# Kernel tuning notes

Hardware: AMD Instinct MI355X
Metric: run time of the kernel (lower is better)

## Reference

```python
import jax, jax.numpy as jnp
import numpy as np

H, DK = 16, 64
D = H * DK  # d_model = 1024
B, S = 2, 2048


def setup_inputs() -> dict:
    key = jax.random.key(0)
    ks = jax.random.split(key, 11)
    std = 1.0 / np.sqrt(D)
    inp = {
        "query": jax.random.normal(ks[0], (B, S, D), dtype=jnp.float32),
        "key": jax.random.normal(ks[1], (B, S, D), dtype=jnp.float32),
        "value": jax.random.normal(ks[2], (B, S, D), dtype=jnp.float32),
        "Wq": jax.random.normal(ks[3], (D, D), dtype=jnp.float32) * std,
        "bq": jnp.zeros((D,), dtype=jnp.float32),
        "Wk": jax.random.normal(ks[4], (D, D), dtype=jnp.float32) * std,
        "bk": jnp.zeros((D,), dtype=jnp.float32),
        "Wv": jax.random.normal(ks[5], (D, D), dtype=jnp.float32) * std,
        "bv": jnp.zeros((D,), dtype=jnp.float32),
        "Wo": jax.random.normal(ks[6], (D, D), dtype=jnp.float32) * std,
        "bo": jnp.zeros((D,), dtype=jnp.float32),
    }
    return inp


def reference(query, key, value, Wq, bq, Wk, bk, Wv, bv, Wo, bo):
    # torch.nn.Linear convention: y = x @ W.T + b
    def split_heads(x):
        b, s, _ = x.shape
        return x.reshape(b, s, H, DK).transpose(0, 2, 1, 3)  # [B,H,S,DK]

    q = split_heads(query @ Wq.T + bq)
    k = split_heads(key @ Wk.T + bk)
    v = split_heads(value @ Wv.T + bv)

    scale = 1.0 / jnp.sqrt(jnp.asarray(DK, dtype=q.dtype))
    scores = jnp.einsum("bhqd,bhkd->bhqk", q, k) * scale  # [B,H,S,S]
    p_attn = jax.nn.softmax(scores, axis=-1)
    ctx = jnp.einsum("bhqk,bhkd->bhqd", p_attn, v)  # [B,H,S,DK]

    ctx = ctx.transpose(0, 2, 1, 3).reshape(query.shape[0], -1, H * DK)
    return ctx @ Wo.T + bo
```

## Files before the change

### kernel.cpp

```cpp
#include <hip/hip_runtime.h>
#include <stdint.h>

#define BATCH 2
#define SEQ   2048
#define NHEAD 16
#define DK    64
#define DMODEL 1024
#define MROWS (BATCH*SEQ)

typedef __attribute__((ext_vector_type(8))) __bf16 bf16x8;
typedef __attribute__((ext_vector_type(4))) float f32x4;
typedef __attribute__((ext_vector_type(8))) unsigned short u16x8;
typedef __attribute__((ext_vector_type(4))) unsigned short u16x4;

#define QSCALE 0.18033688f

__device__ __forceinline__ unsigned short f2bf(float f) {
  union { float f; uint32_t u; } c; c.f = f;
  uint32_t u = c.u;
  return (unsigned short)((u + 0x7fffu + ((u >> 16) & 1u)) >> 16);
}

__device__ __forceinline__ void gld16(const void* g, void* lds) {
  __builtin_amdgcn_global_load_lds(
      (const __attribute__((address_space(1))) void*)g,
      (__attribute__((address_space(3))) void*)lds,
      16, 0, 0);
}

__global__ __launch_bounds__(256)
void cvt_all(const float* __restrict__ q, const float* __restrict__ k, const float* __restrict__ v,
             const float* __restrict__ Wq, const float* __restrict__ Wk,
             const float* __restrict__ Wv, const float* __restrict__ Wo,
             unsigned short* __restrict__ Xq, unsigned short* __restrict__ Xk,
             unsigned short* __restrict__ Xv,
             unsigned short* __restrict__ Wqb, unsigned short* __restrict__ Wkb,
             unsigned short* __restrict__ Wvb, unsigned short* __restrict__ Wob) {
  int blk = blockIdx.x;
  const float* in; unsigned short* out; int base;
  if (blk < 6144) {
    int ti = blk >> 11;
    in  = (ti == 0) ? q  : (ti == 1) ? k  : v;
    out = (ti == 0) ? Xq : (ti == 1) ? Xk : Xv;
    base = (blk & 2047) * 2048;
  } else {
    int ti = (blk - 6144) >> 9;
    in  = (ti == 0) ? Wq  : (ti == 1) ? Wk  : (ti == 2) ? Wv  : Wo;
    out = (ti == 0) ? Wqb : (ti == 1) ? Wkb : (ti == 2) ? Wvb : Wob;
    base = ((blk - 6144) & 511) * 2048;
  }
  int i = base + threadIdx.x * 8;
  float4 a = *(const float4*)(in + i);
  float4 b = *(const float4*)(in + i + 4);
  u16x8 o;
  o[0]=f2bf(a.x); o[1]=f2bf(a.y); o[2]=f2bf(a.z); o[3]=f2bf(a.w);
  o[4]=f2bf(b.x); o[5]=f2bf(b.y); o[6]=f2bf(b.z); o[7]=f2bf(b.w);
  *(u16x8*)(out + i) = o;
}

template <int MODE, int MT>
__device__ __forceinline__ void gemm_body(unsigned short* __restrict__ lA,
                                          unsigned short* __restrict__ lB,
                                          const unsigned short* __restrict__ X,
                                          const unsigned short* __restrict__ W,
                                          const float* __restrict__ bias,
                                          unsigned short* __restrict__ Yb,
                                          float* __restrict__ Yf,
                                          int rowBase, int colBase) {
  const int t = threadIdx.x;
  const int lane = t & 63, wave = t >> 6;
  const int cl = lane & 15, qd = lane >> 4;
  const int wm = wave >> 1, wn = wave & 1;
  const int srow = t >> 3, sslot = t & 7;

  int aoff[2][MT], boff[2][4];
  #pragma unroll
  for (int ks = 0; ks < 2; ks++) {
    #pragma unroll
    for (int i = 0; i < MT; i++) {
      int ra = wm * (MT * 16) + i * 16 + cl;
      aoff[ks][i] = ra * 64 + ((ks * 4 + qd) ^ (ra & 7)) * 8;
    }
    #pragma unroll
    for (int i = 0; i < 4; i++) {
      int rb = wn * 64 + i * 16 + cl;
      boff[ks][i] = rb * 64 + ((ks * 4 + qd) ^ (rb & 7)) * 8;
    }
  }
  const unsigned short* xp[MT];
  const unsigned short* wp[4];
  #pragma unroll
  for (int i = 0; i < MT; i++) {
    int r = i * 32 + srow;
    int chunk = sslot ^ (r & 7);
    xp[i] = X + (size_t)(rowBase + r) * DMODEL + chunk * 8;
  }
  #pragma unroll
  for (int i = 0; i < 4; i++) {
    int r = i * 32 + srow;
    int chunk = sslot ^ (r & 7);
    wp[i] = W + (size_t)(colBase + r) * DMODEL + chunk * 8;
  }

  f32x4 zero = {0.f, 0.f, 0.f, 0.f};
  f32x4 acc[MT][4];
  for (int mt = 0; mt < MT; mt++) for (int nt = 0; nt < 4; nt++) acc[mt][nt] = zero;

  for (int k0 = 0; k0 < DMODEL; k0 += 64) {
    __syncthreads();
    #pragma unroll
    for (int i = 0; i < MT; i++) {
      gld16(xp[i], (char*)lA + i * 4096 + wave * 1024);
      xp[i] += 64;
    }
    #pragma unroll
    for (int i = 0; i < 4; i++) {
      gld16(wp[i], (char*)lB + i * 4096 + wave * 1024);
      wp[i] += 64;
    }
    __syncthreads();
    #pragma unroll
    for (int ks = 0; ks < 2; ks++) {
      bf16x8 af[MT], bfr[4];
      #pragma unroll
      for (int mt = 0; mt < MT; mt++) af[mt] = *(const bf16x8*)&lA[aoff[ks][mt]];
      #pragma unroll
      for (int nt = 0; nt < 4; nt++) bfr[nt] = *(const bf16x8*)&lB[boff[ks][nt]];
      #pragma unroll
      for (int mt = 0; mt < MT; mt++)
        #pragma unroll
        for (int nt = 0; nt < 4; nt++) {
          if (MODE == 2)
            acc[mt][nt] = __builtin_amdgcn_mfma_f32_16x16x32_bf16(af[mt], bfr[nt], acc[mt][nt], 0, 0, 0);
          else
            acc[mt][nt] = __builtin_amdgcn_mfma_f32_16x16x32_bf16(bfr[nt], af[mt], acc[mt][nt], 0, 0, 0);
        }
    }
  }

  if (MODE == 2) {
    #pragma unroll
    for (int mt = 0; mt < MT; mt++) {
      int row0 = rowBase + wm * (MT * 16) + mt * 16 + qd * 4;
      int bb = row0 >> 11;
      int s_in = row0 & 2047;
      int blk = s_in & ~63;
      int n4 = (s_in & 63) >> 2;
      int l4 = n4 & 7;
      int pos = 8 * (n4 >> 3) + ((l4 < 4) ? 2 * l4 : 2 * (l4 - 4) + 1);
      #pragma unroll
      for (int nt = 0; nt < 4; nt++) {
        int c = colBase + wn * 64 + nt * 16 + cl;
        float bv = bias[c];
        int hh = c >> 6, d = c & 63;
        u16x4 v;
        #pragma unroll
        for (int r = 0; r < 4; r++) v[r] = f2bf(acc[mt][nt][r] + bv);
        *(u16x4*)&Yb[(size_t)((bb * NHEAD + hh) * 64 + d) * SEQ + blk + pos * 4] = v;
      }
    }
  } else {
    #pragma unroll
    for (int nt = 0; nt < 4; nt++) {
      int col = colBase + wn * 64 + nt * 16 + qd * 4;
      f32x4 bv4 = *(const f32x4*)&bias[col];
      #pragma unroll
      for (int mt = 0; mt < MT; mt++) {
        int row = rowBase + wm * (MT * 16) + mt * 16 + cl;
        if (MODE == 3) {
          f32x4 v;
          #pragma unroll
          for (int r = 0; r < 4; r++) v[r] = acc[mt][nt][r] + bv4[r];
          *(f32x4*)&Yf[(size_t)row * DMODEL + col] = v;
        } else {
          u16x4 v;
          #pragma unroll
          for (int r = 0; r < 4; r++) {
            float x = acc[mt][nt][r] + bv4[r];
            v[r] = f2bf(MODE == 1 ? x * QSCALE : x);
          }
          *(u16x4*)&Yb[(size_t)row * DMODEL + col] = v;
        }
      }
    }
  }
}

__global__ __launch_bounds__(256)
void gemm_qkv(const unsigned short* __restrict__ Xq, const unsigned short* __restrict__ Xk,
              const unsigned short* __restrict__ Xv,
              const unsigned short* __restrict__ Wq, const unsigned short* __restrict__ Wk,
              const unsigned short* __restrict__ Wv,
              const float* __restrict__ bq, const float* __restrict__ bk,
              const float* __restrict__ bv,
              unsigned short* __restrict__ Q, unsigned short* __restrict__ K,
              unsigned short* __restrict__ VT) {
  __shared__ unsigned short lA[64 * 64];
  __shared__ unsigned short lB[128 * 64];
  int id = blockIdx.x;
  int by = id & 63, bx = id >> 6;
  int z = blockIdx.z;
  if (z == 0)      gemm_body<1, 2>(lA, lB, Xq, Wq, bq, Q,  nullptr, by * 64, bx * 128);
  else if (z == 1) gemm_body<0, 2>(lA, lB, Xk, Wk, bk, K,  nullptr, by * 64, bx * 128);
  else             gemm_body<2, 2>(lA, lB, Xv, Wv, bv, VT, nullptr, by * 64, bx * 128);
}

__global__ __launch_bounds__(256)
void gemm_out(const unsigned short* __restrict__ CTX, const unsigned short* __restrict__ Wo,
              const float* __restrict__ bo, float* __restrict__ out) {
  __shared__ unsigned short lA[64 * 64];
  __shared__ unsigned short lB[128 * 64];
  int id = blockIdx.x;
  int by = id & 63, bx = id >> 6;
  gemm_body<3, 2>(lA, lB, CTX, Wo, bo, nullptr, out, by * 64, bx * 128);
}

__global__ __launch_bounds__(256)
void attn(const unsigned short* __restrict__ Q, const unsigned short* __restrict__ K,
          const unsigned short* __restrict__ VT, unsigned short* __restrict__ CTX) {
  __shared__ unsigned short lK[2 * 64 * 64];
  __shared__ unsigned short lV[2 * 64 * 64];
  const int t = threadIdx.x, lane = t & 63, wave = t >> 6;
  const int cl = lane & 15, qd = lane >> 4;
  const int flat = blockIdx.x + 16 * blockIdx.y + 256 * blockIdx.z;
  const int loc = flat >> 3;
  const int p = (flat & 7) * 4 + (loc >> 4);
  const int qt = loc & 15, h = p & 15, b = p >> 4;
  const int srow = t >> 3, sslot = t & 7;

  #pragma unroll
  for (int half = 0; half < 2; half++)
    #pragma unroll
    for (int i = 0; i < 2; i++) {
      int r = i * 32 + srow;
      int chunk = sslot ^ (r & 7);
      gld16(Q + (size_t)(b * SEQ + qt * 128 + half * 64 + r) * DMODEL + h * 64 + chunk * 8,
            (char*)lK + half * 8192 + i * 4096 + wave * 1024);
    }
  __syncthreads();
  bf16x8 qf[2][2];
  #pragma unroll
  for (int qg = 0; qg < 2; qg++)
    #pragma unroll
    for (int ks = 0; ks < 2; ks++) {
      int r = wave * 16 + cl;
      int slot = (ks * 4 + qd) ^ (r & 7);
      qf[qg][ks] = *(const bf16x8*)&lK[qg * 4096 + r * 64 + slot * 8];
    }
  __syncthreads();

  int ka[8], va[8];
  #pragma unroll
  for (int ks = 0; ks < 2; ks++)
    #pragma unroll
    for (int nt = 0; nt < 4; nt++) {
      int rk = nt * 16 + cl;
      ka[ks * 4 + nt] = rk * 64 + ((ks * 4 + qd) ^ (rk & 7)) * 8;
    }
  #pragma unroll
  for (int ntp = 0; ntp < 2; ntp++)
    #pragma unroll
    for (int dt = 0; dt < 4; dt++) {
      int d = dt * 16 + cl;
      va[ntp * 4 + dt] = d * 64 + ((4 * ntp + qd) ^ (d & 7)) * 8;
    }

  const unsigned short* kp[2];
  const unsigned short* vp[2];
  #pragma unroll
  for (int i = 0; i < 2; i++) {
    int r = i * 32 + srow;
    int chunk = sslot ^ (r & 7);
    kp[i] = K + (size_t)(b * SEQ + r) * DMODEL + h * 64 + chunk * 8;
    vp[i] = VT + (size_t)((b * NHEAD + h) * 64 + r) * SEQ + chunk * 8;
    gld16(kp[i], (char*)lK + i * 4096 + wave * 1024);
    gld16(vp[i], (char*)lV + i * 4096 + wave * 1024);
    kp[i] += 64 * DMODEL; vp[i] += 64;
  }

  f32x4 zero = {0.f, 0.f, 0.f, 0.f};
  f32x4 o[2][4];
  f32x4 osum[2];
  #pragma unroll
  for (int qg = 0; qg < 2; qg++) {
    #pragma unroll
    for (int dt = 0; dt < 4; dt++) o[qg][dt] = zero;
    osum[qg] = zero;
  }
  bf16x8 ones;
  #pragma unroll
  for (int j = 0; j < 8; j++) ones[j] = (__bf16)1.0f;

  #pragma unroll 2
  for (int kt = 0; kt < SEQ / 64; kt++) {
    const int cb = (kt & 1) * 4096;
    __syncthreads();
    if (kt + 1 < SEQ / 64) {
      const int nb = ((kt + 1) & 1) * 8192;
      #pragma unroll
      for (int i = 0; i < 2; i++) {
        gld16(kp[i], (char*)lK + nb + i * 4096 + wave * 1024);
        gld16(vp[i], (char*)lV + nb + i * 4096 + wave * 1024);
        kp[i] += 64 * DMODEL; vp[i] += 64;
      }
    }

    f32x4 sc[2][4];
    #pragma unroll
    for (int qg = 0; qg < 2; qg++)
      #pragma unroll
      for (int nt = 0; nt < 4; nt++) sc[qg][nt] = zero;
    #pragma unroll
    for (int ks = 0; ks < 2; ks++)
      #pragma unroll
      for (int nt = 0; nt < 4; nt++) {
        bf16x8 kf = *(const bf16x8*)&lK[cb + ka[ks * 4 + nt]];
        sc[0][nt] = __builtin_amdgcn_mfma_f32_16x16x32_bf16(kf, qf[0][ks], sc[0][nt], 0, 0, 0);
        sc[1][nt] = __builtin_amdgcn_mfma_f32_16x16x32_bf16(kf, qf[1][ks], sc[1][nt], 0, 0, 0);
      }

    bf16x8 pb[2][2];
    #pragma unroll
    for (int qg = 0; qg < 2; qg++)
      #pragma unroll
      for (int ntp = 0; ntp < 2; ntp++) {
        bf16x8 x;
        #pragma unroll
        for (int j = 0; j < 4; j++)
          x[j] = (__bf16)__builtin_amdgcn_exp2f(sc[qg][2 * ntp][j]);
        #pragma unroll
        for (int j = 0; j < 4; j++)
          x[4 + j] = (__bf16)__builtin_amdgcn_exp2f(sc[qg][2 * ntp + 1][j]);
        pb[qg][ntp] = x;
      }

    #pragma unroll
    for (int qg = 0; qg < 2; qg++) {
      osum[qg] = __builtin_amdgcn_mfma_f32_16x16x32_bf16(ones, pb[qg][0], osum[qg], 0, 0, 0);
      osum[qg] = __builtin_amdgcn_mfma_f32_16x16x32_bf16(ones, pb[qg][1], osum[qg], 0, 0, 0);
    }

    #pragma unroll
    for (int ntp = 0; ntp < 2; ntp++)
      #pragma unroll
      for (int dt = 0; dt < 4; dt++) {
        bf16x8 vf = *(const bf16x8*)&lV[cb + va[ntp * 4 + dt]];
        o[0][dt] = __builtin_amdgcn_mfma_f32_16x16x32_bf16(vf, pb[0][ntp], o[0][dt], 0, 0, 0);
        o[1][dt] = __builtin_amdgcn_mfma_f32_16x16x32_bf16(vf, pb[1][ntp], o[1][dt], 0, 0, 0);
      }
  }

  #pragma unroll
  for (int qg = 0; qg < 2; qg++) {
    float inv = 1.f / osum[qg][0];
    int row = b * SEQ + qt * 128 + qg * 64 + wave * 16 + cl;
    #pragma unroll
    for (int dt = 0; dt < 4; dt++) {
      u16x4 v;
      #pragma unroll
      for (int r = 0; r < 4; r++) v[r] = f2bf(o[qg][dt][r] * inv);
      *(u16x4*)&CTX[(size_t)row * DMODEL + h * 64 + dt * 16 + qd * 4] = v;
    }
  }
}

extern "C" void kernel_launch(void* const* d_in, const int* in_sizes, int n_in,
                              void* d_out, int out_size, void* d_ws, size_t ws_size,
                              hipStream_t stream) {
  const float* q  = (const float*)d_in[0];
  const float* k  = (const float*)d_in[1];
  const float* v  = (const float*)d_in[2];
  const float* Wq = (const float*)d_in[3]; const float* bq = (const float*)d_in[4];
  const float* Wk = (const float*)d_in[5]; const float* bk = (const float*)d_in[6];
  const float* Wv = (const float*)d_in[7]; const float* bv = (const float*)d_in[8];
  const float* Wo = (const float*)d_in[9]; const float* bo = (const float*)d_in[10];
  float* out = (float*)d_out;

  char* ws = (char*)d_ws;
  const size_t MB = 1u << 20;
  unsigned short* Xq  = (unsigned short*)(ws + 0 * MB);
  unsigned short* Xk  = (unsigned short*)(ws + 8 * MB);
  unsigned short* Xv  = (unsigned short*)(ws + 16 * MB);
  unsigned short* Wqb = (unsigned short*)(ws + 24 * MB);
  unsigned short* Wkb = (unsigned short*)(ws + 26 * MB);
  unsigned short* Wvb = (unsigned short*)(ws + 28 * MB);
  unsigned short* Wob = (unsigned short*)(ws + 70 * MB);
  unsigned short* Qp  = (unsigned short*)(ws + 32 * MB);
  unsigned short* Kp  = (unsigned short*)(ws + 40 * MB);
  unsigned short* VT  = (unsigned short*)(ws + 48 * MB);
  unsigned short* CTX = (unsigned short*)(ws + 56 * MB);

  cvt_all<<<8192, 256, 0, stream>>>(q, k, v, Wq, Wk, Wv, Wo,
                                    Xq, Xk, Xv, Wqb, Wkb, Wvb, Wob);

  gemm_qkv<<<dim3(512, 1, 3), 256, 0, stream>>>(
      Xq, Xk, Xv, Wqb, Wkb, Wvb, bq, bk, bv, Qp, Kp, VT);

  attn<<<dim3(SEQ / 128, NHEAD, BATCH), 256, 0, stream>>>(Qp, Kp, VT, CTX);

  gemm_out<<<512, 256, 0, stream>>>(CTX, Wob, bo, out);
}
```

Measured before the change: 208.3 us.

## Fuse fp32-to-bf16 activation conversion into QKV GEMM A-tile loads

The separate conversion pass over the query, key and value activations is removed. The QKV GEMM now loads fp32 activation tiles straight into LDS using a new swizzle and converts them to bf16 in registers before the MFMA. This saves one full write and re-read of 24MB of bf16 intermediates. In exchange the GEMM moves twice as many A-tile bytes from global memory, uses more LDS, and does conversion work inside its inner loop, where it is repeated for each column block.

```diff
diff --git a/kernel.cpp b/kernel.cpp
--- a/kernel.cpp
+++ b/kernel.cpp
@@ -29,27 +29,15 @@
 }
 
 __global__ __launch_bounds__(256)
-void cvt_all(const float* __restrict__ q, const float* __restrict__ k, const float* __restrict__ v,
-             const float* __restrict__ Wq, const float* __restrict__ Wk,
-             const float* __restrict__ Wv, const float* __restrict__ Wo,
-             unsigned short* __restrict__ Xq, unsigned short* __restrict__ Xk,
-             unsigned short* __restrict__ Xv,
-             unsigned short* __restrict__ Wqb, unsigned short* __restrict__ Wkb,
-             unsigned short* __restrict__ Wvb, unsigned short* __restrict__ Wob) {
+void cvt_w(const float* __restrict__ Wq, const float* __restrict__ Wk,
+           const float* __restrict__ Wv, const float* __restrict__ Wo,
+           unsigned short* __restrict__ Wqb, unsigned short* __restrict__ Wkb,
+           unsigned short* __restrict__ Wvb, unsigned short* __restrict__ Wob) {
   int blk = blockIdx.x;
-  const float* in; unsigned short* out; int base;
-  if (blk < 6144) {
-    int ti = blk >> 11;
-    in  = (ti == 0) ? q  : (ti == 1) ? k  : v;
-    out = (ti == 0) ? Xq : (ti == 1) ? Xk : Xv;
-    base = (blk & 2047) * 2048;
-  } else {
-    int ti = (blk - 6144) >> 9;
-    in  = (ti == 0) ? Wq  : (ti == 1) ? Wk  : (ti == 2) ? Wv  : Wo;
-    out = (ti == 0) ? Wqb : (ti == 1) ? Wkb : (ti == 2) ? Wvb : Wob;
-    base = ((blk - 6144) & 511) * 2048;
-  }
-  int i = base + threadIdx.x * 8;
+  int ti = blk >> 9;
+  const float* in  = (ti == 0) ? Wq  : (ti == 1) ? Wk  : (ti == 2) ? Wv  : Wo;
+  unsigned short* out = (ti == 0) ? Wqb : (ti == 1) ? Wkb : (ti == 2) ? Wvb : Wob;
+  int i = (blk & 511) * 2048 + threadIdx.x * 8;
   float4 a = *(const float4*)(in + i);
   float4 b = *(const float4*)(in + i + 4);
   u16x8 o;
@@ -58,10 +46,12 @@
   *(u16x8*)(out + i) = o;
 }
 
-template <int MODE, int MT>
+template <int MODE, int MT, bool AF32>
 __device__ __forceinline__ void gemm_body(unsigned short* __restrict__ lA,
+                                          float* __restrict__ lAf,
                                           unsigned short* __restrict__ lB,
                                           const unsigned short* __restrict__ X,
+                                          const float* __restrict__ Xf,
                                           const unsigned short* __restrict__ W,
                                           const float* __restrict__ bias,
                                           unsigned short* __restrict__ Yb,
@@ -79,7 +69,12 @@
     #pragma unroll
     for (int i = 0; i < MT; i++) {
       int ra = wm * (MT * 16) + i * 16 + cl;
-      aoff[ks][i] = ra * 64 + ((ks * 4 + qd) ^ (ra & 7)) * 8;
+      if constexpr (AF32) {
+        int s0 = (8 * ks + 2 * qd) ^ (ra & 15);
+        aoff[ks][i] = ra * 64 + s0 * 4;
+      } else {
+        aoff[ks][i] = ra * 64 + ((ks * 4 + qd) ^ (ra & 7)) * 8;
+      }
     }
     #pragma unroll
     for (int i = 0; i < 4; i++) {
@@ -88,12 +83,22 @@
     }
   }
   const unsigned short* xp[MT];
+  const float* xpf[2 * MT];
   const unsigned short* wp[4];
-  #pragma unroll
-  for (int i = 0; i < MT; i++) {
-    int r = i * 32 + srow;
-    int chunk = sslot ^ (r & 7);
-    xp[i] = X + (size_t)(rowBase + r) * DMODEL + chunk * 8;
+  if constexpr (AF32) {
+    #pragma unroll
+    for (int i = 0; i < 2 * MT; i++) {
+      int r = i * 16 + (t >> 4);
+      int gc = (t & 15) ^ (r & 15);
+      xpf[i] = Xf + (size_t)(rowBase + r) * DMODEL + gc * 4;
+    }
+  } else {
+    #pragma unroll
+    for (int i = 0; i < MT; i++) {
+      int r = i * 32 + srow;
+      int chunk = sslot ^ (r & 7);
+      xp[i] = X + (size_t)(rowBase + r) * DMODEL + chunk * 8;
+    }
   }
   #pragma unroll
   for (int i = 0; i < 4; i++) {
@@ -108,10 +113,18 @@
 
   for (int k0 = 0; k0 < DMODEL; k0 += 64) {
     __syncthreads();
-    #pragma unroll
-    for (int i = 0; i < MT; i++) {
-      gld16(xp[i], (char*)lA + i * 4096 + wave * 1024);
-      xp[i] += 64;
+    if constexpr (AF32) {
+      #pragma unroll
+      for (int i = 0; i < 2 * MT; i++) {
+        gld16(xpf[i], (char*)lAf + i * 4096 + wave * 1024);
+        xpf[i] += 64;
+      }
+    } else {
+      #pragma unroll
+      for (int i = 0; i < MT; i++) {
+        gld16(xp[i], (char*)lA + i * 4096 + wave * 1024);
+        xp[i] += 64;
+      }
     }
     #pragma unroll
     for (int i = 0; i < 4; i++) {
@@ -123,7 +136,18 @@
     for (int ks = 0; ks < 2; ks++) {
       bf16x8 af[MT], bfr[4];
       #pragma unroll
-      for (int mt = 0; mt < MT; mt++) af[mt] = *(const bf16x8*)&lA[aoff[ks][mt]];
+      for (int mt = 0; mt < MT; mt++) {
+        if constexpr (AF32) {
+          f32x4 a0 = *(const f32x4*)&lAf[aoff[ks][mt]];
+          f32x4 a1 = *(const f32x4*)&lAf[aoff[ks][mt] ^ 4];
+          bf16x8 x;
+          #pragma unroll
+          for (int j = 0; j < 4; j++) { x[j] = (__bf16)a0[j]; x[4 + j] = (__bf16)a1[j]; }
+          af[mt] = x;
+        } else {
+          af[mt] = *(const bf16x8*)&lA[aoff[ks][mt]];
+        }
+      }
       #pragma unroll
       for (int nt = 0; nt < 4; nt++) bfr[nt] = *(const bf16x8*)&lB[boff[ks][nt]];
       #pragma unroll
@@ -187,22 +211,22 @@
 }
 
 __global__ __launch_bounds__(256)
-void gemm_qkv(const unsigned short* __restrict__ Xq, const unsigned short* __restrict__ Xk,
-              const unsigned short* __restrict__ Xv,
+void gemm_qkv(const float* __restrict__ q, const float* __restrict__ k,
+              const float* __restrict__ v,
               const unsigned short* __restrict__ Wq, const unsigned short* __restrict__ Wk,
               const unsigned short* __restrict__ Wv,
               const float* __restrict__ bq, const float* __restrict__ bk,
               const float* __restrict__ bv,
               unsigned short* __restrict__ Q, unsigned short* __restrict__ K,
               unsigned short* __restrict__ VT) {
-  __shared__ unsigned short lA[64 * 64];
+  __shared__ float lAf[64 * 64];
   __shared__ unsigned short lB[128 * 64];
   int id = blockIdx.x;
   int by = id & 63, bx = id >> 6;
   int z = blockIdx.z;
-  if (z == 0)      gemm_body<1, 2>(lA, lB, Xq, Wq, bq, Q,  nullptr, by * 64, bx * 128);
-  else if (z == 1) gemm_body<0, 2>(lA, lB, Xk, Wk, bk, K,  nullptr, by * 64, bx * 128);
-  else             gemm_body<2, 2>(lA, lB, Xv, Wv, bv, VT, nullptr, by * 64, bx * 128);
+  if (z == 0)      gemm_body<1, 2, true>(nullptr, lAf, lB, nullptr, q, Wq, bq, Q,  nullptr, by * 64, bx * 128);
+  else if (z == 1) gemm_body<0, 2, true>(nullptr, lAf, lB, nullptr, k, Wk, bk, K,  nullptr, by * 64, bx * 128);
+  else             gemm_body<2, 2, true>(nullptr, lAf, lB, nullptr, v, Wv, bv, VT, nullptr, by * 64, bx * 128);
 }
 
 __global__ __launch_bounds__(256)
@@ -212,7 +236,7 @@
   __shared__ unsigned short lB[128 * 64];
   int id = blockIdx.x;
   int by = id & 63, bx = id >> 6;
-  gemm_body<3, 2>(lA, lB, CTX, Wo, bo, nullptr, out, by * 64, bx * 128);
+  gemm_body<3, 2, false>(lA, nullptr, lB, CTX, nullptr, Wo, bo, nullptr, out, by * 64, bx * 128);
 }
 
 __global__ __launch_bounds__(256)
@@ -378,9 +402,6 @@
 
   char* ws = (char*)d_ws;
   const size_t MB = 1u << 20;
-  unsigned short* Xq  = (unsigned short*)(ws + 0 * MB);
-  unsigned short* Xk  = (unsigned short*)(ws + 8 * MB);
-  unsigned short* Xv  = (unsigned short*)(ws + 16 * MB);
   unsigned short* Wqb = (unsigned short*)(ws + 24 * MB);
   unsigned short* Wkb = (unsigned short*)(ws + 26 * MB);
   unsigned short* Wvb = (unsigned short*)(ws + 28 * MB);
@@ -390,11 +411,10 @@
   unsigned short* VT  = (unsigned short*)(ws + 48 * MB);
   unsigned short* CTX = (unsigned short*)(ws + 56 * MB);
 
-  cvt_all<<<8192, 256, 0, stream>>>(q, k, v, Wq, Wk, Wv, Wo,
-                                    Xq, Xk, Xv, Wqb, Wkb, Wvb, Wob);
+  cvt_w<<<2048, 256, 0, stream>>>(Wq, Wk, Wv, Wo, Wqb, Wkb, Wvb, Wob);
 
   gemm_qkv<<<dim3(512, 1, 3), 256, 0, stream>>>(
-      Xq, Xk, Xv, Wqb, Wkb, Wvb, bq, bk, bv, Qp, Kp, VT);
+      q, k, v, Wqb, Wkb, Wvb, bq, bk, bv, Qp, Kp, VT);
 
   attn<<<dim3(SEQ / 128, NHEAD, BATCH), 256, 0, stream>>>(Qp, Kp, VT, CTX);
 
```

New measurement: 222.1 us. 6.6% more time.
